# Kernel optimization log

Measured on AMD Instinct MI355X. Metric: run time of the kernel, lower is better.

Reference implementation:

```python
import jax, jax.numpy as jnp
import numpy as np

N_NODES = 50000

def _gat_layer(x, src, dst, W, a_l, a_r, bias, alpha, agg, act, n_nodes):
    # x: [N, in]; W: [in, H*F]; a_l, a_r: [H, F]; bias: [H*F]
    H, F = a_l.shape
    z = (x @ W).reshape(n_nodes, H, F)                      # [N,H,F]
    el = jnp.einsum('nhf,hf->nh', z, a_l)                   # [N,H]
    er = jnp.einsum('nhf,hf->nh', z, a_r)                   # [N,H]
    e = jax.nn.leaky_relu(el[src] + er[dst], alpha)         # [E,H]
    # segment softmax over in-edges of each destination node
    m = jax.ops.segment_max(e, dst, num_segments=n_nodes)   # [N,H]
    ex = jnp.exp(e - m[dst])                                # [E,H]
    s = jax.ops.segment_sum(ex, dst, num_segments=n_nodes)  # [N,H]
    attn = ex / jnp.maximum(s[dst], 1e-9)                   # [E,H]
    msg = attn[:, :, None] * z[src]                         # [E,H,F]
    h = jax.ops.segment_sum(msg, dst, num_segments=n_nodes) # [N,H,F]
    # identity residual (in_feats == H*F) as in DGL GATConv
    h = h + x.reshape(n_nodes, -1, F)
    h = h + bias.reshape(1, H, F)
    if agg == 'flatten':
        h = h.reshape(n_nodes, H * F)
    else:  # mean over heads
        h = h.mean(axis=1)
    if act is not None:
        h = act(h)
    return h


def setup_inputs() -> dict:
    key = jax.random.key(0)
    ks = jax.random.split(key, 14)
    N, E, D = N_NODES, 800000, 128
    H, F = 4, 32
    sc_in = 1.0 / np.sqrt(D)
    sc_h = 1.0 / np.sqrt(H * F)
    inp = {
        'feats': jax.random.normal(ks[0], (N, D), jnp.float32),
        'src': jax.random.randint(ks[1], (E,), 0, N),
        'dst': jax.random.randint(ks[2], (E,), 0, N),
        'W1': jax.random.normal(ks[3], (D, H * F), jnp.float32) * sc_in,
        'al1': jax.random.normal(ks[4], (H, F), jnp.float32) * sc_h,
        'ar1': jax.random.normal(ks[5], (H, F), jnp.float32) * sc_h,
        'b1': jnp.zeros((H * F,), jnp.float32),
        'W2': jax.random.normal(ks[6], (H * F, H * F), jnp.float32) * sc_h,
        'al2': jax.random.normal(ks[7], (H, F), jnp.float32) * sc_h,
        'ar2': jax.random.normal(ks[8], (H, F), jnp.float32) * sc_h,
        'b2': jnp.zeros((H * F,), jnp.float32),
        'Wp': jax.random.normal(ks[9], (F, 1), jnp.float32) / np.sqrt(F),
        'bp': jnp.zeros((1,), jnp.float32),
    }
    return inp


def reference(feats, src, dst, W1, al1, ar1, b1, W2, al2, ar2, b2, Wp, bp):
    h = _gat_layer(feats, src, dst, W1, al1, ar1, b1, 0.2, 'flatten', jax.nn.elu, N_NODES)
    h = _gat_layer(h, src, dst, W2, al2, ar2, b2, 0.2, 'mean', None, N_NODES)
    return h @ Wp + bp  # [N, 1]
```

## Files before the change

### kernel.cpp

```cpp
#include <hip/hip_runtime.h>
#include <hip/hip_bf16.h>

#define NN 50000
#define NE 800000
#define HF 128

#define OFF_FLAG   0u
#define OFF_ROWPTR 256u
#define OFF_BSUM   200272u
#define OFF_BOFF   200480u
#define OFF_DEG    200704u
#define OFF_FILL   400896u
#define OFF_ADJ    601088u
#define OFF_FX     3801088u
#define OFF_WC1    16601088u
#define OFF_WC2    16633856u
#define OFF_PAR    16666624u
#define OFF_Z      16668672u
#define OFF_H1     29468672u
#define OFF_EL     42268672u
#define OFF_ER     43068672u

typedef __hip_bfloat16 bf16;
typedef unsigned short us16;

#define N_SMALL 33569

#define PREP_RANK_B   3125
#define PREP_FEATS_B  6250
#define PREP_SMALL_B  132
#define PREP_GRID     (PREP_RANK_B + PREP_FEATS_B + PREP_SMALL_B)

typedef __attribute__((ext_vector_type(8))) short bf16x8;
typedef __attribute__((ext_vector_type(4))) float f32x4;

__device__ __forceinline__ float us2f(us16 u) {
  union { unsigned int i; float f; } c; c.i = ((unsigned int)u) << 16; return c.f;
}
__device__ __forceinline__ us16 f2us(float f) {
  bf16 h = __float2bfloat16(f);
  union { bf16 h; us16 u; } c; c.h = h; return c.u;
}
__device__ __forceinline__ float blo(unsigned v) {
  union { unsigned i; float f; } c; c.i = v << 16; return c.f;
}
__device__ __forceinline__ float bhi(unsigned v) {
  union { unsigned i; float f; } c; c.i = v & 0xffff0000u; return c.f;
}
__device__ __forceinline__ unsigned pk2(float a, float b) {
  return (unsigned)f2us(a) | ((unsigned)f2us(b) << 16);
}

__device__ __forceinline__ int detect_f32(const us16* __restrict__ u) {
  int t = threadIdx.x;
  int mx = 0;
  for (int i = t; i < 2048; i += 256) {
    int e = (u[i] >> 7) & 0xFF;
    mx = mx > e ? mx : e;
  }
#pragma unroll
  for (int m = 32; m >= 1; m >>= 1) {
    int o = __shfl_xor(mx, m);
    mx = mx > o ? mx : o;
  }
  __shared__ int sred[4];
  if ((t & 63) == 0) sred[t >> 6] = mx;
  __syncthreads();
  int a = sred[0] > sred[1] ? sred[0] : sred[1];
  int b = sred[2] > sred[3] ? sred[2] : sred[3];
  int r = a > b ? a : b;
  return r >= 135;
}

__global__ __launch_bounds__(256) void k_prep(
    const void* __restrict__ feats, us16* __restrict__ fx,
    const void* s0, const void* s1, const void* s2, const void* s3, const void* s4,
    const void* s5, const void* s6, const void* s7, const void* s8, const void* s9,
    us16* d0, us16* d1, us16* d2, us16* d3, us16* d4,
    us16* d5, us16* d6, us16* d7, us16* d8, us16* d9,
    const int* __restrict__ dst, int* __restrict__ fillp, int* __restrict__ rank,
    int* __restrict__ flag) {
  int b = blockIdx.x;
  if (b < PREP_RANK_B) {
    int e = b * 256 + threadIdx.x;
    if (e < NE) rank[e] = atomicAdd(&fillp[dst[e] * 16], 1);
    return;
  }
  int f = detect_f32((const us16*)s0);
  if (b == PREP_RANK_B && threadIdx.x == 0) *flag = f;
  if (b < PREP_RANK_B + PREP_FEATS_B) {
    int i = ((b - PREP_RANK_B) * 256 + threadIdx.x) * 4;
    if (f) {
      float4 v = *(const float4*)((const float*)feats + i);
      ushort4 o;
      o.x = f2us(v.x); o.y = f2us(v.y); o.z = f2us(v.z); o.w = f2us(v.w);
      *(ushort4*)(fx + i) = o;
    } else {
      *(ushort4*)(fx + i) = *(const ushort4*)((const us16*)feats + i);
    }
  } else {
    const void* sp[10] = {s0, s1, s2, s3, s4, s5, s6, s7, s8, s9};
    us16* dp[10] = {d0, d1, d2, d3, d4, d5, d6, d7, d8, d9};
    const int cnt[10] = {16384, 16384, 128, 128, 128, 128, 128, 128, 32, 1};
    int gid = (b - PREP_RANK_B - PREP_FEATS_B) * 256 + threadIdx.x;
    int base = 0;
#pragma unroll
    for (int p = 0; p < 10; ++p) {
      int loc = gid - base;
      if (loc >= 0 && loc < cnt[p])
        dp[p][loc] = f ? f2us(((const float*)sp[p])[loc]) : ((const us16*)sp[p])[loc];
      base += cnt[p];
    }
  }
}

__global__ __launch_bounds__(1024) void k_s1(const int* __restrict__ fillp,
                                             int* __restrict__ bsum) {
  __shared__ int red[1024];
  int t = threadIdx.x;
  int i = blockIdx.x * 1024 + t;
  red[t] = (i < NN) ? fillp[i * 16] : 0;
  __syncthreads();
  for (int s = 512; s > 0; s >>= 1) {
    if (t < s) red[t] += red[t + s];
    __syncthreads();
  }
  if (t == 0) bsum[blockIdx.x] = red[0];
}

__global__ __launch_bounds__(64) void k_s2(const int* __restrict__ bsum,
                                           int* __restrict__ boff,
                                           int* __restrict__ rowptr) {
  int lane = threadIdx.x;
  const int NB = (NN + 1023) / 1024;
  int v = (lane < NB) ? bsum[lane] : 0;
  int orig = v;
#pragma unroll
  for (int off = 1; off < 64; off <<= 1) {
    int u = __shfl_up(v, off);
    if (lane >= off) v += u;
  }
  if (lane < NB) boff[lane] = v - orig;
  if (lane == 0) rowptr[NN] = NE;
}

__global__ __launch_bounds__(1024) void k_s3(const int* __restrict__ fillp,
                                             const int* __restrict__ boff,
                                             int* __restrict__ rowptr) {
  __shared__ int part[1024];
  int t = threadIdx.x;
  int i = blockIdx.x * 1024 + t;
  int d = (i < NN) ? fillp[i * 16] : 0;
  part[t] = d;
  __syncthreads();
  for (int off = 1; off < 1024; off <<= 1) {
    int v = (t >= off) ? part[t - off] : 0;
    __syncthreads();
    part[t] += v;
    __syncthreads();
  }
  if (i < NN) rowptr[i] = boff[blockIdx.x] + part[t] - d;
}

__global__ void k_place(const int* __restrict__ src, const int* __restrict__ dst,
                        const int* __restrict__ rowptr, const int* __restrict__ rank,
                        int* __restrict__ adj) {
  int e = blockIdx.x * 256 + threadIdx.x;
  if (e < NE) adj[rowptr[dst[e]] + rank[e]] = src[e];
}

__global__ __launch_bounds__(256) void k_gemm(const us16* __restrict__ X,
                                              const us16* __restrict__ W,
                                              us16* __restrict__ Z,
                                              const us16* __restrict__ al,
                                              const us16* __restrict__ ar,
                                              float* __restrict__ el,
                                              float* __restrict__ er) {
  __shared__ us16 Wl[HF * HF];
  int tid = threadIdx.x;
  for (int e = tid; e < HF * HF; e += 256) {
    int k = e >> 7, n = e & 127;
    int d = ((((k >> 5) * 8 + (n >> 4)) * 4 + ((k >> 3) & 3)) * 16 + (n & 15)) * 8 + (k & 7);
    Wl[d] = W[e];
  }
  __syncthreads();

  int w = tid >> 6;
  int lane = tid & 63;
  int q = lane >> 4;
  int c = lane & 15;
  int m0 = blockIdx.x * 64 + w * 16;

  int rA = m0 + c;
  if (rA >= NN) rA = NN - 1;
  const us16* xrow = X + (size_t)rA * HF;

  f32x4 acc[8] = {};
#pragma unroll
  for (int s = 0; s < 4; ++s) {
    bf16x8 a = *(const bf16x8*)&xrow[s * 32 + q * 8];
#pragma unroll
    for (int t = 0; t < 8; ++t) {
      bf16x8 b = *(const bf16x8*)&Wl[((((s * 8) + t) * 4 + q) * 16 + c) * 8];
      acc[t] = __builtin_amdgcn_mfma_f32_16x16x32_bf16(a, b, acc[t], 0, 0, 0);
    }
  }

#pragma unroll
  for (int reg = 0; reg < 4; ++reg) {
    int row = m0 + q * 4 + reg;
    if (row < NN) {
      us16* zrow = Z + (size_t)row * HF;
#pragma unroll
      for (int t = 0; t < 8; ++t) zrow[t * 16 + c] = f2us(acc[t][reg]);
    }
  }

  float alv[8], arv[8];
#pragma unroll
  for (int t = 0; t < 8; ++t) {
    alv[t] = us2f(al[t * 16 + c]);
    arv[t] = us2f(ar[t * 16 + c]);
  }
#pragma unroll
  for (int reg = 0; reg < 4; ++reg) {
    int row = m0 + q * 4 + reg;
    float pl[4], pr[4];
#pragma unroll
    for (int h = 0; h < 4; ++h) {
      pl[h] = acc[2 * h][reg] * alv[2 * h] + acc[2 * h + 1][reg] * alv[2 * h + 1];
      pr[h] = acc[2 * h][reg] * arv[2 * h] + acc[2 * h + 1][reg] * arv[2 * h + 1];
    }
#pragma unroll
    for (int m = 1; m < 16; m <<= 1) {
#pragma unroll
      for (int h = 0; h < 4; ++h) {
        pl[h] += __shfl_xor(pl[h], m);
        pr[h] += __shfl_xor(pr[h], m);
      }
    }
    if (row < NN) {
      int cc = c & 3;
      float vl = cc == 0 ? pl[0] : cc == 1 ? pl[1] : cc == 2 ? pl[2] : pl[3];
      float vr = cc == 0 ? pr[0] : cc == 1 ? pr[1] : cc == 2 ? pr[2] : pr[3];
      if (c < 4) el[row * 4 + cc] = vl;
      else if (c < 8) er[row * 4 + cc] = vr;
    }
  }
}

template <int LAYER>
__global__ __launch_bounds__(256) void k_agg(
    const us16* __restrict__ Z, const float* __restrict__ el,
    const float* __restrict__ er, const int* __restrict__ rowptr,
    const int* __restrict__ adj, const us16* __restrict__ resid,
    const us16* __restrict__ bias, us16* __restrict__ Hout,
    const us16* __restrict__ Wp, const us16* __restrict__ bp,
    void* __restrict__ out, const int* __restrict__ flag) {
  int n = blockIdx.x * 4 + (threadIdx.x >> 6);
  int lane = threadIdx.x & 63;
  int g = lane >> 4;
  int p = lane & 15;
  int hl = p >> 2;
  int f0 = p * 8;
  int begin = rowptr[n];
  int deg = rowptr[n + 1] - begin;
  float erh = er[n * 4 + hl];

  float acc[8] = {};
  float ssum = 0.f;
  int i = g;
  for (; i + 4 < deg; i += 8) {
    int s0 = adj[begin + i];
    int s1 = adj[begin + i + 4];
    float l0 = el[s0 * 4 + hl];
    float l1 = el[s1 * 4 + hl];
    uint4 za = *(const uint4*)&Z[(size_t)s0 * HF + f0];
    uint4 zb = *(const uint4*)&Z[(size_t)s1 * HF + f0];
    float sc0 = l0 + erh; sc0 = sc0 > 0.f ? sc0 : 0.2f * sc0;
    float sc1 = l1 + erh; sc1 = sc1 > 0.f ? sc1 : 0.2f * sc1;
    float ex0 = __expf(sc0);
    float ex1 = __expf(sc1);
    ssum += ex0 + ex1;
    acc[0] = fmaf(ex0, blo(za.x), acc[0]); acc[1] = fmaf(ex0, bhi(za.x), acc[1]);
    acc[2] = fmaf(ex0, blo(za.y), acc[2]); acc[3] = fmaf(ex0, bhi(za.y), acc[3]);
    acc[4] = fmaf(ex0, blo(za.z), acc[4]); acc[5] = fmaf(ex0, bhi(za.z), acc[5]);
    acc[6] = fmaf(ex0, blo(za.w), acc[6]); acc[7] = fmaf(ex0, bhi(za.w), acc[7]);
    acc[0] = fmaf(ex1, blo(zb.x), acc[0]); acc[1] = fmaf(ex1, bhi(zb.x), acc[1]);
    acc[2] = fmaf(ex1, blo(zb.y), acc[2]); acc[3] = fmaf(ex1, bhi(zb.y), acc[3]);
    acc[4] = fmaf(ex1, blo(zb.z), acc[4]); acc[5] = fmaf(ex1, bhi(zb.z), acc[5]);
    acc[6] = fmaf(ex1, blo(zb.w), acc[6]); acc[7] = fmaf(ex1, bhi(zb.w), acc[7]);
  }
  if (i < deg) {
    int s = adj[begin + i];
    float sc = el[s * 4 + hl] + erh;
    sc = sc > 0.f ? sc : 0.2f * sc;
    float ex = __expf(sc);
    ssum += ex;
    uint4 zq = *(const uint4*)&Z[(size_t)s * HF + f0];
    acc[0] = fmaf(ex, blo(zq.x), acc[0]); acc[1] = fmaf(ex, bhi(zq.x), acc[1]);
    acc[2] = fmaf(ex, blo(zq.y), acc[2]); acc[3] = fmaf(ex, bhi(zq.y), acc[3]);
    acc[4] = fmaf(ex, blo(zq.z), acc[4]); acc[5] = fmaf(ex, bhi(zq.z), acc[5]);
    acc[6] = fmaf(ex, blo(zq.w), acc[6]); acc[7] = fmaf(ex, bhi(zq.w), acc[7]);
  }
  ssum += __shfl_xor(ssum, 16); ssum += __shfl_xor(ssum, 32);
#pragma unroll
  for (int j = 0; j < 8; ++j) {
    acc[j] += __shfl_xor(acc[j], 16);
    acc[j] += __shfl_xor(acc[j], 32);
  }
  float inv = 1.f / fmaxf(ssum, 1e-9f);

  uint4 xq = *(const uint4*)&resid[(size_t)n * HF + f0];
  uint4 bq = *(const uint4*)&bias[f0];
  float t0 = fmaf(acc[0], inv, blo(xq.x) + blo(bq.x));
  float t1 = fmaf(acc[1], inv, bhi(xq.x) + bhi(bq.x));
  float t2 = fmaf(acc[2], inv, blo(xq.y) + blo(bq.y));
  float t3 = fmaf(acc[3], inv, bhi(xq.y) + bhi(bq.y));
  float t4 = fmaf(acc[4], inv, blo(xq.z) + blo(bq.z));
  float t5 = fmaf(acc[5], inv, bhi(xq.z) + bhi(bq.z));
  float t6 = fmaf(acc[6], inv, blo(xq.w) + blo(bq.w));
  float t7 = fmaf(acc[7], inv, bhi(xq.w) + bhi(bq.w));

  if (LAYER == 1) {
    t0 = t0 > 0.f ? t0 : __expf(t0) - 1.f;
    t1 = t1 > 0.f ? t1 : __expf(t1) - 1.f;
    t2 = t2 > 0.f ? t2 : __expf(t2) - 1.f;
    t3 = t3 > 0.f ? t3 : __expf(t3) - 1.f;
    t4 = t4 > 0.f ? t4 : __expf(t4) - 1.f;
    t5 = t5 > 0.f ? t5 : __expf(t5) - 1.f;
    t6 = t6 > 0.f ? t6 : __expf(t6) - 1.f;
    t7 = t7 > 0.f ? t7 : __expf(t7) - 1.f;
    if (g == 0) {
      uint4 o;
      o.x = pk2(t0, t1); o.y = pk2(t2, t3); o.z = pk2(t4, t5); o.w = pk2(t6, t7);
      *(uint4*)&Hout[(size_t)n * HF + f0] = o;
    }
  } else {
    t0 += __shfl_xor(t0, 4); t0 += __shfl_xor(t0, 8);
    t1 += __shfl_xor(t1, 4); t1 += __shfl_xor(t1, 8);
    t2 += __shfl_xor(t2, 4); t2 += __shfl_xor(t2, 8);
    t3 += __shfl_xor(t3, 4); t3 += __shfl_xor(t3, 8);
    t4 += __shfl_xor(t4, 4); t4 += __shfl_xor(t4, 8);
    t5 += __shfl_xor(t5, 4); t5 += __shfl_xor(t5, 8);
    t6 += __shfl_xor(t6, 4); t6 += __shfl_xor(t6, 8);
    t7 += __shfl_xor(t7, 4); t7 += __shfl_xor(t7, 8);
    int fw = (p & 3) * 8;
    float pr = 0.25f * (t0 * us2f(Wp[fw]) + t1 * us2f(Wp[fw + 1]) +
                        t2 * us2f(Wp[fw + 2]) + t3 * us2f(Wp[fw + 3]) +
                        t4 * us2f(Wp[fw + 4]) + t5 * us2f(Wp[fw + 5]) +
                        t6 * us2f(Wp[fw + 6]) + t7 * us2f(Wp[fw + 7]));
    pr += __shfl_xor(pr, 1); pr += __shfl_xor(pr, 2);
    if (lane == 0) {
      float res = pr + us2f(bp[0]);
      if (*flag) ((float*)out)[n] = res;
      else ((us16*)out)[n] = f2us(res);
    }
  }
}

extern "C" void kernel_launch(void* const* d_in, const int* in_sizes, int n_in,
                              void* d_out, int out_size, void* d_ws, size_t ws_size,
                              hipStream_t stream) {
  const int* src = (const int*)d_in[1];
  const int* dst = (const int*)d_in[2];
  char* ws = (char*)d_ws;
  int* flag   = (int*)(ws + OFF_FLAG);
  int* rowptr = (int*)(ws + OFF_ROWPTR);
  int* bsum   = (int*)(ws + OFF_BSUM);
  int* boff   = (int*)(ws + OFF_BOFF);
  int* adj    = (int*)(ws + OFF_ADJ);
  us16* fx    = (us16*)(ws + OFF_FX);
  us16* wc1   = (us16*)(ws + OFF_WC1);
  us16* wc2   = (us16*)(ws + OFF_WC2);
  us16* al1   = (us16*)(ws + OFF_PAR + 0);
  us16* ar1   = (us16*)(ws + OFF_PAR + 256);
  us16* b1    = (us16*)(ws + OFF_PAR + 512);
  us16* al2   = (us16*)(ws + OFF_PAR + 768);
  us16* ar2   = (us16*)(ws + OFF_PAR + 1024);
  us16* b2    = (us16*)(ws + OFF_PAR + 1280);
  us16* wp    = (us16*)(ws + OFF_PAR + 1536);
  us16* bp    = (us16*)(ws + OFF_PAR + 1792);
  us16* z     = (us16*)(ws + OFF_Z);
  us16* h1    = (us16*)(ws + OFF_H1);
  float* el   = (float*)(ws + OFF_EL);
  float* er   = (float*)(ws + OFF_ER);
  int* rank   = (int*)(ws + OFF_Z);
  int* fillp  = (int*)(ws + OFF_H1);

  const int NB = (NN + 1023) / 1024;

  hipMemsetAsync(fillp, 0, (size_t)NN * 16 * 4, stream);

  hipLaunchKernelGGL(k_prep, dim3(PREP_GRID), dim3(256), 0, stream,
                     d_in[0], fx,
                     d_in[3], d_in[7], d_in[4], d_in[5], d_in[6],
                     d_in[8], d_in[9], d_in[10], d_in[11], d_in[12],
                     wc1, wc2, al1, ar1, b1, al2, ar2, b2, wp, bp,
                     dst, fillp, rank, flag);

  hipLaunchKernelGGL(k_s1, dim3(NB), dim3(1024), 0, stream, fillp, bsum);
  hipLaunchKernelGGL(k_s2, dim3(1), dim3(64), 0, stream, bsum, boff, rowptr);
  hipLaunchKernelGGL(k_s3, dim3(NB), dim3(1024), 0, stream, fillp, boff, rowptr);
  hipLaunchKernelGGL(k_place, dim3(3125), dim3(256), 0, stream, src, dst, rowptr, rank, adj);

  hipLaunchKernelGGL(k_gemm, dim3((NN + 63) / 64), dim3(256), 0, stream, fx, wc1, z,
                     al1, ar1, el, er);
  hipLaunchKernelGGL((k_agg<1>), dim3(NN / 4), dim3(256), 0, stream, z, el, er, rowptr, adj,
                     fx, b1, h1, (us16*)nullptr, (us16*)nullptr, (void*)nullptr, flag);
  hipLaunchKernelGGL(k_gemm, dim3((NN + 63) / 64), dim3(256), 0, stream, h1, wc2, z,
                     al2, ar2, el, er);
  hipLaunchKernelGGL((k_agg<2>), dim3(NN / 4), dim3(256), 0, stream, z, el, er, rowptr, adj,
                     h1, b2, (us16*)nullptr, wp, bp, d_out, flag);
}
```

Baseline: 254.5 us.

## Merge scan kernels with grid sync and fuse edge placement with layer-one GEMM

Replaces the three prefix-scan kernels with a single kernel in which block 0 waits on an atomic counter, scans the block sums and releases the other blocks through a flag. The edge-placement kernel and the first GEMM are merged into one launch with split block roles, and rank moves to its own buffer so it no longer overlaps Z. The aim is to cut launch gaps and let the placement and GEMM work overlap. The spin-wait grid sync assumes all 49 blocks are resident at once, which risks deadlock if they are not.

```diff
diff --git a/kernel.cpp b/kernel.cpp
--- a/kernel.cpp
+++ b/kernel.cpp
@@ -9,8 +9,7 @@
 #define OFF_ROWPTR 256u
 #define OFF_BSUM   200272u
 #define OFF_BOFF   200480u
-#define OFF_DEG    200704u
-#define OFF_FILL   400896u
+#define OFF_SYNC   200680u
 #define OFF_ADJ    601088u
 #define OFF_FX     3801088u
 #define OFF_WC1    16601088u
@@ -20,16 +19,19 @@
 #define OFF_H1     29468672u
 #define OFF_EL     42268672u
 #define OFF_ER     43068672u
+#define OFF_RANK   50000128u
 
 typedef __hip_bfloat16 bf16;
 typedef unsigned short us16;
-
-#define N_SMALL 33569
 
 #define PREP_RANK_B   3125
 #define PREP_FEATS_B  6250
 #define PREP_SMALL_B  132
 #define PREP_GRID     (PREP_RANK_B + PREP_FEATS_B + PREP_SMALL_B)
+
+#define NB_SCAN 49
+#define GP_PLACE_B 3125
+#define GEMM_B 782
 
 typedef __attribute__((ext_vector_type(8))) short bf16x8;
 typedef __attribute__((ext_vector_type(4))) float f32x4;
@@ -79,8 +81,9 @@
     us16* d0, us16* d1, us16* d2, us16* d3, us16* d4,
     us16* d5, us16* d6, us16* d7, us16* d8, us16* d9,
     const int* __restrict__ dst, int* __restrict__ fillp, int* __restrict__ rank,
-    int* __restrict__ flag) {
+    int* __restrict__ flag, int* __restrict__ sync) {
   int b = blockIdx.x;
+  if (b == 0 && threadIdx.x == 0) { sync[0] = 0; sync[1] = 0; }
   if (b < PREP_RANK_B) {
     int e = b * 256 + threadIdx.x;
     if (e < NE) rank[e] = atomicAdd(&fillp[dst[e] * 16], 1);
@@ -114,42 +117,14 @@
   }
 }
 
-__global__ __launch_bounds__(1024) void k_s1(const int* __restrict__ fillp,
-                                             int* __restrict__ bsum) {
-  __shared__ int red[1024];
-  int t = threadIdx.x;
-  int i = blockIdx.x * 1024 + t;
-  red[t] = (i < NN) ? fillp[i * 16] : 0;
-  __syncthreads();
-  for (int s = 512; s > 0; s >>= 1) {
-    if (t < s) red[t] += red[t + s];
-    __syncthreads();
-  }
-  if (t == 0) bsum[blockIdx.x] = red[0];
-}
-
-__global__ __launch_bounds__(64) void k_s2(const int* __restrict__ bsum,
-                                           int* __restrict__ boff,
-                                           int* __restrict__ rowptr) {
-  int lane = threadIdx.x;
-  const int NB = (NN + 1023) / 1024;
-  int v = (lane < NB) ? bsum[lane] : 0;
-  int orig = v;
-#pragma unroll
-  for (int off = 1; off < 64; off <<= 1) {
-    int u = __shfl_up(v, off);
-    if (lane >= off) v += u;
-  }
-  if (lane < NB) boff[lane] = v - orig;
-  if (lane == 0) rowptr[NN] = NE;
-}
-
-__global__ __launch_bounds__(1024) void k_s3(const int* __restrict__ fillp,
-                                             const int* __restrict__ boff,
-                                             int* __restrict__ rowptr) {
+__global__ __launch_bounds__(1024) void k_scanall(const int* __restrict__ fillp,
+                                                  int* __restrict__ bsum,
+                                                  int* __restrict__ boff,
+                                                  int* __restrict__ rowptr,
+                                                  int* __restrict__ sync) {
   __shared__ int part[1024];
-  int t = threadIdx.x;
-  int i = blockIdx.x * 1024 + t;
+  int t = threadIdx.x, b = blockIdx.x;
+  int i = b * 1024 + t;
   int d = (i < NN) ? fillp[i * 16] : 0;
   part[t] = d;
   __syncthreads();
@@ -159,14 +134,136 @@
     part[t] += v;
     __syncthreads();
   }
-  if (i < NN) rowptr[i] = boff[blockIdx.x] + part[t] - d;
-}
-
-__global__ void k_place(const int* __restrict__ src, const int* __restrict__ dst,
-                        const int* __restrict__ rowptr, const int* __restrict__ rank,
-                        int* __restrict__ adj) {
-  int e = blockIdx.x * 256 + threadIdx.x;
-  if (e < NE) adj[rowptr[dst[e]] + rank[e]] = src[e];
+  int incl = part[t];
+  if (t == 1023) {
+    bsum[b] = incl;
+    __threadfence();
+    atomicAdd(&sync[0], 1);
+  }
+  if (b == 0) {
+    __syncthreads();
+    if (t == 0) {
+      while (atomicAdd(&sync[0], 0) < NB_SCAN) { }
+    }
+    __syncthreads();
+    if (t < 64) {
+      int v = (t < NB_SCAN) ? bsum[t] : 0;
+      int orig = v;
+#pragma unroll
+      for (int off = 1; off < 64; off <<= 1) {
+        int u = __shfl_up(v, off);
+        if (t >= off) v += u;
+      }
+      if (t < NB_SCAN) boff[t] = v - orig;
+      if (t == 0) rowptr[NN] = NE;
+    }
+    __syncthreads();
+    if (t == 0) {
+      __threadfence();
+      atomicExch(&sync[1], 1);
+    }
+  }
+  if (t == 0) {
+    while (atomicAdd(&sync[1], 0) == 0) { }
+  }
+  __syncthreads();
+  if (i < NN) rowptr[i] = boff[b] + incl - d;
+}
+
+__device__ __forceinline__ void gemm_body(const us16* __restrict__ X,
+                                          const us16* __restrict__ W,
+                                          us16* __restrict__ Z,
+                                          const us16* __restrict__ al,
+                                          const us16* __restrict__ ar,
+                                          float* __restrict__ el,
+                                          float* __restrict__ er, int blk) {
+  __shared__ us16 Wl[HF * HF];
+  int tid = threadIdx.x;
+  for (int e = tid; e < HF * HF; e += 256) {
+    int k = e >> 7, n = e & 127;
+    int d = ((((k >> 5) * 8 + (n >> 4)) * 4 + ((k >> 3) & 3)) * 16 + (n & 15)) * 8 + (k & 7);
+    Wl[d] = W[e];
+  }
+  __syncthreads();
+
+  int w = tid >> 6;
+  int lane = tid & 63;
+  int q = lane >> 4;
+  int c = lane & 15;
+  int m0 = blk * 64 + w * 16;
+
+  int rA = m0 + c;
+  if (rA >= NN) rA = NN - 1;
+  const us16* xrow = X + (size_t)rA * HF;
+
+  f32x4 acc[8] = {};
+#pragma unroll
+  for (int s = 0; s < 4; ++s) {
+    bf16x8 a = *(const bf16x8*)&xrow[s * 32 + q * 8];
+#pragma unroll
+    for (int t = 0; t < 8; ++t) {
+      bf16x8 bb = *(const bf16x8*)&Wl[((((s * 8) + t) * 4 + q) * 16 + c) * 8];
+      acc[t] = __builtin_amdgcn_mfma_f32_16x16x32_bf16(a, bb, acc[t], 0, 0, 0);
+    }
+  }
+
+#pragma unroll
+  for (int reg = 0; reg < 4; ++reg) {
+    int row = m0 + q * 4 + reg;
+    if (row < NN) {
+      us16* zrow = Z + (size_t)row * HF;
+#pragma unroll
+      for (int t = 0; t < 8; ++t) zrow[t * 16 + c] = f2us(acc[t][reg]);
+    }
+  }
+
+  float alv[8], arv[8];
+#pragma unroll
+  for (int t = 0; t < 8; ++t) {
+    alv[t] = us2f(al[t * 16 + c]);
+    arv[t] = us2f(ar[t * 16 + c]);
+  }
+#pragma unroll
+  for (int reg = 0; reg < 4; ++reg) {
+    int row = m0 + q * 4 + reg;
+    float pl[4], pr[4];
+#pragma unroll
+    for (int h = 0; h < 4; ++h) {
+      pl[h] = acc[2 * h][reg] * alv[2 * h] + acc[2 * h + 1][reg] * alv[2 * h + 1];
+      pr[h] = acc[2 * h][reg] * arv[2 * h] + acc[2 * h + 1][reg] * arv[2 * h + 1];
+    }
+#pragma unroll
+    for (int m = 1; m < 16; m <<= 1) {
+#pragma unroll
+      for (int h = 0; h < 4; ++h) {
+        pl[h] += __shfl_xor(pl[h], m);
+        pr[h] += __shfl_xor(pr[h], m);
+      }
+    }
+    if (row < NN) {
+      int cc = c & 3;
+      float vl = cc == 0 ? pl[0] : cc == 1 ? pl[1] : cc == 2 ? pl[2] : pl[3];
+      float vr = cc == 0 ? pr[0] : cc == 1 ? pr[1] : cc == 2 ? pr[2] : pr[3];
+      if (c < 4) el[row * 4 + cc] = vl;
+      else if (c < 8) er[row * 4 + cc] = vr;
+    }
+  }
+}
+
+__global__ __launch_bounds__(256) void k_gemmplace(
+    const us16* __restrict__ X, const us16* __restrict__ W, us16* __restrict__ Z,
+    const us16* __restrict__ al, const us16* __restrict__ ar,
+    float* __restrict__ el, float* __restrict__ er,
+    const int* __restrict__ src, const int* __restrict__ dst,
+    const int* __restrict__ rowptr, const int* __restrict__ rank,
+    int* __restrict__ adj) {
+  int b = blockIdx.x;
+  if (b < GP_PLACE_B) {
+    int e = b * 256 + threadIdx.x;
+    if (e < NE) adj[rowptr[dst[e]] + rank[e]] = src[e];
+    return;
+  }
+  gemm_body(X, W, Z, al, ar, el, er, b - GP_PLACE_B);
 }
 
 __global__ __launch_bounds__(256) void k_gemm(const us16* __restrict__ X,
@@ -176,77 +273,7 @@
                                               const us16* __restrict__ ar,
                                               float* __restrict__ el,
                                               float* __restrict__ er) {
-  __shared__ us16 Wl[HF * HF];
-  int tid = threadIdx.x;
-  for (int e = tid; e < HF * HF; e += 256) {
-    int k = e >> 7, n = e & 127;
-    int d = ((((k >> 5) * 8 + (n >> 4)) * 4 + ((k >> 3) & 3)) * 16 + (n & 15)) * 8 + (k & 7);
-    Wl[d] = W[e];
-  }
-  __syncthreads();
-
-  int w = tid >> 6;
-  int lane = tid & 63;
-  int q = lane >> 4;
-  int c = lane & 15;
-  int m0 = blockIdx.x * 64 + w * 16;
-
-  int rA = m0 + c;
-  if (rA >= NN) rA = NN - 1;
-  const us16* xrow = X + (size_t)rA * HF;
-
-  f32x4 acc[8] = {};
-#pragma unroll
-  for (int s = 0; s < 4; ++s) {
-    bf16x8 a = *(const bf16x8*)&xrow[s * 32 + q * 8];
-#pragma unroll
-    for (int t = 0; t < 8; ++t) {
-      bf16x8 b = *(const bf16x8*)&Wl[((((s * 8) + t) * 4 + q) * 16 + c) * 8];
-      acc[t] = __builtin_amdgcn_mfma_f32_16x16x32_bf16(a, b, acc[t], 0, 0, 0);
-    }
-  }
-
-#pragma unroll
-  for (int reg = 0; reg < 4; ++reg) {
-    int row = m0 + q * 4 + reg;
-    if (row < NN) {
-      us16* zrow = Z + (size_t)row * HF;
-#pragma unroll
-      for (int t = 0; t < 8; ++t) zrow[t * 16 + c] = f2us(acc[t][reg]);
-    }
-  }
-
-  float alv[8], arv[8];
-#pragma unroll
-  for (int t = 0; t < 8; ++t) {
-    alv[t] = us2f(al[t * 16 + c]);
-    arv[t] = us2f(ar[t * 16 + c]);
-  }
-#pragma unroll
-  for (int reg = 0; reg < 4; ++reg) {
-    int row = m0 + q * 4 + reg;
-    float pl[4], pr[4];
-#pragma unroll
-    for (int h = 0; h < 4; ++h) {
-      pl[h] = acc[2 * h][reg] * alv[2 * h] + acc[2 * h + 1][reg] * alv[2 * h + 1];
-      pr[h] = acc[2 * h][reg] * arv[2 * h] + acc[2 * h + 1][reg] * arv[2 * h + 1];
-    }
-#pragma unroll
-    for (int m = 1; m < 16; m <<= 1) {
-#pragma unroll
-      for (int h = 0; h < 4; ++h) {
-        pl[h] += __shfl_xor(pl[h], m);
-        pr[h] += __shfl_xor(pr[h], m);
-      }
-    }
-    if (row < NN) {
-      int cc = c & 3;
-      float vl = cc == 0 ? pl[0] : cc == 1 ? pl[1] : cc == 2 ? pl[2] : pl[3];
-      float vr = cc == 0 ? pr[0] : cc == 1 ? pr[1] : cc == 2 ? pr[2] : pr[3];
-      if (c < 4) el[row * 4 + cc] = vl;
-      else if (c < 8) er[row * 4 + cc] = vr;
-    }
-  }
+  gemm_body(X, W, Z, al, ar, el, er, blockIdx.x);
 }
 
 template <int LAYER>
@@ -369,6 +396,7 @@
   int* rowptr = (int*)(ws + OFF_ROWPTR);
   int* bsum   = (int*)(ws + OFF_BSUM);
   int* boff   = (int*)(ws + OFF_BOFF);
+  int* sync   = (int*)(ws + OFF_SYNC);
   int* adj    = (int*)(ws + OFF_ADJ);
   us16* fx    = (us16*)(ws + OFF_FX);
   us16* wc1   = (us16*)(ws + OFF_WC1);
@@ -385,10 +413,8 @@
   us16* h1    = (us16*)(ws + OFF_H1);
   float* el   = (float*)(ws + OFF_EL);
   float* er   = (float*)(ws + OFF_ER);
-  int* rank   = (int*)(ws + OFF_Z);
   int* fillp  = (int*)(ws + OFF_H1);
-
-  const int NB = (NN + 1023) / 1024;
+  int* rank   = (int*)(ws + OFF_RANK);
 
   hipMemsetAsync(fillp, 0, (size_t)NN * 16 * 4, stream);
 
@@ -397,18 +423,17 @@
                      d_in[3], d_in[7], d_in[4], d_in[5], d_in[6],
                      d_in[8], d_in[9], d_in[10], d_in[11], d_in[12],
                      wc1, wc2, al1, ar1, b1, al2, ar2, b2, wp, bp,
-                     dst, fillp, rank, flag);
-
-  hipLaunchKernelGGL(k_s1, dim3(NB), dim3(1024), 0, stream, fillp, bsum);
-  hipLaunchKernelGGL(k_s2, dim3(1), dim3(64), 0, stream, bsum, boff, rowptr);
-  hipLaunchKernelGGL(k_s3, dim3(NB), dim3(1024), 0, stream, fillp, boff, rowptr);
-  hipLaunchKernelGGL(k_place, dim3(3125), dim3(256), 0, stream, src, dst, rowptr, rank, adj);
-
-  hipLaunchKernelGGL(k_gemm, dim3((NN + 63) / 64), dim3(256), 0, stream, fx, wc1, z,
-                     al1, ar1, el, er);
+                     dst, fillp, rank, flag, sync);
+
+  hipLaunchKernelGGL(k_scanall, dim3(NB_SCAN), dim3(1024), 0, stream,
+                     fillp, bsum, boff, rowptr, sync);
+
+  hipLaunchKernelGGL(k_gemmplace, dim3(GP_PLACE_B + GEMM_B), dim3(256), 0, stream,
+                     fx, wc1, z, al1, ar1, el, er, src, dst, rowptr, rank, adj);
+
   hipLaunchKernelGGL((k_agg<1>), dim3(NN / 4), dim3(256), 0, stream, z, el, er, rowptr, adj,
                      fx, b1, h1, (us16*)nullptr, (us16*)nullptr, (void*)nullptr, flag);
-  hipLaunchKernelGGL(k_gemm, dim3((NN + 63) / 64), dim3(256), 0, stream, h1, wc2, z,
+  hipLaunchKernelGGL(k_gemm, dim3(GEMM_B), dim3(256), 0, stream, h1, wc2, z,
                      al2, ar2, el, er);
   hipLaunchKernelGGL((k_agg<2>), dim3(NN / 4), dim3(256), 0, stream, z, el, er, rowptr, adj,
                      h1, b2, (us16*)nullptr, wp, bp, d_out, flag);
```

Result: no change. 250.7 us (-1.5%).
